# Performance work log

Measured on AMD Instinct MI355X. Metric: run time of the kernel, lower is better.

## Reference

```python
import jax, jax.numpy as jnp
import numpy as np

N_SRC = 100000
N_DST = 100000
N_EDGES = 1250000
D_FEAT = 64
HIDDEN = 64
OUT = 128


def setup_inputs() -> dict:
    key = jax.random.key(0)
    ks = jax.random.split(key, 9)
    h_src = jax.random.normal(ks[0], (N_SRC, D_FEAT), dtype=jnp.float32)
    h_dst = jax.random.normal(ks[1], (N_DST, D_FEAT), dtype=jnp.float32)
    edge_weight = jax.random.uniform(ks[2], (N_EDGES,), dtype=jnp.float32)
    W1 = jax.random.normal(ks[3], (D_FEAT, HIDDEN), dtype=jnp.float32) / np.sqrt(D_FEAT)
    b1 = jnp.zeros((HIDDEN,), dtype=jnp.float32)
    W2 = jax.random.normal(ks[4], (HIDDEN + D_FEAT, OUT), dtype=jnp.float32) / np.sqrt(HIDDEN + D_FEAT)
    b2 = jnp.zeros((OUT,), dtype=jnp.float32)
    src_idx = jax.random.randint(ks[5], (N_EDGES,), 0, N_SRC, dtype=jnp.int32)
    dst_idx = jax.random.randint(ks[6], (N_EDGES,), 0, N_DST, dtype=jnp.int32)
    return {
        "h_src": h_src, "h_dst": h_dst, "edge_weight": edge_weight,
        "W1": W1, "b1": b1, "W2": W2, "b2": b2,
        "src_idx": src_idx, "dst_idx": dst_idx,
    }


def reference(h_src, h_dst, edge_weight, W1, b1, W2, b2, src_idx, dst_idx):
    # fc_1 with relu on source features: [N_src, H]
    hs = jax.nn.relu(h_src @ W1 + b1)
    # u_mul_e -> sum: edge-weighted scatter-sum into dst nodes
    msg = hs[src_idx] * edge_weight[:, None]                      # [E, H]
    vs = jax.ops.segment_sum(msg, dst_idx, num_segments=N_DST)    # [N_dst, H]
    # copy_e -> sum: per-dst sum of edge weights
    ws = jax.ops.segment_sum(edge_weight, dst_idx, num_segments=N_DST)  # [N_dst]
    ws = jnp.clip(ws, 1.0, None)[:, None]
    nv = vs / ws
    # fc_2 on concat([weighted-mean, h_dst]) with relu
    new = jax.nn.relu(jnp.concatenate([nv, h_dst], axis=-1) @ W2 + b2)
    # global L2 normalization (tf.norm over the full tensor)
    return new / jnp.linalg.norm(new)
```

## Files before the change

### kernel.cpp

```cpp
#include <hip/hip_runtime.h>

#define N_SRC   100000
#define N_DST   100000
#define N_EDGES 1250000
#define D_FEAT  64
#define HIDDEN  64
#define OUT_F   128

#define DPB    128
#define NBUK   782
#define NBLKA  160
#define CHUNK  ((N_EDGES + NBLKA - 1) / NBLKA)
#define NCNT   (NBUK * NBLKA)
#define NB_SC  ((NCNT + 511) / 512)
#define CAPD   2048
#define NT_FC1 782
#define NT_A   391
#define NT_C   (NT_FC1 - NT_A)

struct FC1SM {
    float Xs[128][33];
    float Ws[32][64];
};

__device__ __forceinline__ void fc1_tile(FC1SM& sm, int tile,
        const float* __restrict__ h_src, const float* __restrict__ W1,
        const float* __restrict__ b1, float* __restrict__ hs) {
    const int t  = threadIdx.x;
    const int tr = t >> 3;
    const int tc = t & 7;
    const int base = tile * 128;
    float acc[4][8] = {};

    #pragma unroll 1
    for (int kc = 0; kc < 2; ++kc) {
        const int koff = kc * 32;
        #pragma unroll
        for (int i = 0; i < 4; ++i) {
            int fid = i * 256 + t;
            int row = fid >> 3, q = fid & 7;
            int grow = base + row;
            float4 v = make_float4(0.f, 0.f, 0.f, 0.f);
            if (grow < N_SRC)
                v = *(const float4*)&h_src[(size_t)grow * 64 + koff + q * 4];
            sm.Xs[row][q * 4 + 0] = v.x; sm.Xs[row][q * 4 + 1] = v.y;
            sm.Xs[row][q * 4 + 2] = v.z; sm.Xs[row][q * 4 + 3] = v.w;
        }
        #pragma unroll
        for (int i = 0; i < 2; ++i) {
            int fid = i * 256 + t;
            int kk = fid >> 4, q = fid & 15;
            float4 v = *(const float4*)&W1[(size_t)(koff + kk) * HIDDEN + q * 4];
            *(float4*)&sm.Ws[kk][q * 4] = v;
        }
        __syncthreads();
        #pragma unroll 2
        for (int k = 0; k < 32; ++k) {
            float xv[4];
            #pragma unroll
            for (int r = 0; r < 4; ++r) xv[r] = sm.Xs[tr * 4 + r][k];
            const float4 wlo = *(const float4*)&sm.Ws[k][tc * 8];
            const float4 whi = *(const float4*)&sm.Ws[k][tc * 8 + 4];
            #pragma unroll
            for (int r = 0; r < 4; ++r) {
                acc[r][0] = fmaf(xv[r], wlo.x, acc[r][0]);
                acc[r][1] = fmaf(xv[r], wlo.y, acc[r][1]);
                acc[r][2] = fmaf(xv[r], wlo.z, acc[r][2]);
                acc[r][3] = fmaf(xv[r], wlo.w, acc[r][3]);
                acc[r][4] = fmaf(xv[r], whi.x, acc[r][4]);
                acc[r][5] = fmaf(xv[r], whi.y, acc[r][5]);
                acc[r][6] = fmaf(xv[r], whi.z, acc[r][6]);
                acc[r][7] = fmaf(xv[r], whi.w, acc[r][7]);
            }
        }
        __syncthreads();
    }
    #pragma unroll
    for (int r = 0; r < 4; ++r) {
        int grow = base + tr * 4 + r;
        if (grow < N_SRC) {
            #pragma unroll
            for (int j = 0; j < 8; ++j)
                hs[(size_t)grow * 64 + tc * 8 + j] =
                    fmaxf(acc[r][j] + b1[tc * 8 + j], 0.0f);
        }
    }
}

__global__ __launch_bounds__(256, 4) void fusedA_kernel(
        const int* __restrict__ dst, int* __restrict__ bcnt,
        const float* __restrict__ h_src, const float* __restrict__ W1,
        const float* __restrict__ b1, float* __restrict__ hs) {
    __shared__ union { int h[NBUK]; FC1SM g; } sm;
    if (blockIdx.x >= NBLKA) {
        fc1_tile(sm.g, blockIdx.x - NBLKA, h_src, W1, b1, hs);
        return;
    }
    for (int i = threadIdx.x; i < NBUK; i += 256) sm.h[i] = 0;
    __syncthreads();
    const int lo = blockIdx.x * CHUNK;
    const int hi = min(lo + CHUNK, N_EDGES);
    for (int i = lo + threadIdx.x; i < hi; i += 256)
        atomicAdd(&sm.h[dst[i] >> 7], 1);
    __syncthreads();
    for (int b = threadIdx.x; b < NBUK; b += 256)
        bcnt[b * NBLKA + blockIdx.x] = sm.h[b];
}

__global__ __launch_bounds__(256) void scan_bsum_kernel(
        const int* __restrict__ c, int* __restrict__ bsum, int n) {
    const int t  = threadIdx.x;
    const int i0 = blockIdx.x * 512 + 2 * t;
    int v0 = (i0     < n) ? c[i0]     : 0;
    int v1 = (i0 + 1 < n) ? c[i0 + 1] : 0;
    int s = v0 + v1;
    #pragma unroll
    for (int off = 32; off > 0; off >>= 1) s += __shfl_down(s, off, 64);
    __shared__ int ws[4];
    if ((t & 63) == 0) ws[t >> 6] = s;
    __syncthreads();
    if (t == 0) bsum[blockIdx.x] = ws[0] + ws[1] + ws[2] + ws[3];
}

__global__ __launch_bounds__(256) void scan_boff_kernel(
        const int* __restrict__ bsum, int* __restrict__ boff, int nb) {
    const int t = threadIdx.x, lane = t & 63, w = t >> 6;
    int v = (t < nb) ? bsum[t] : 0;
    int inc = v;
    #pragma unroll
    for (int off = 1; off < 64; off <<= 1) {
        int u = __shfl_up(inc, off, 64);
        if (lane >= off) inc += u;
    }
    __shared__ int wsum[4];
    if (lane == 63) wsum[w] = inc;
    __syncthreads();
    int add = 0;
    for (int i = 0; i < w; ++i) add += wsum[i];
    if (t < nb) boff[t] = add + inc - v;
}

__global__ __launch_bounds__(256) void scan_write_kernel(
        const int* __restrict__ boff, int* __restrict__ c, int n) {
    const int t = threadIdx.x, lane = t & 63, w = t >> 6;
    const int i0 = blockIdx.x * 512 + 2 * t;
    int v0 = (i0     < n) ? c[i0]     : 0;
    int v1 = (i0 + 1 < n) ? c[i0 + 1] : 0;
    int s = v0 + v1;
    int inc = s;
    #pragma unroll
    for (int off = 1; off < 64; off <<= 1) {
        int u = __shfl_up(inc, off, 64);
        if (lane >= off) inc += u;
    }
    __shared__ int wsum[4];
    if (lane == 63) wsum[w] = inc;
    __syncthreads();
    int add = boff[blockIdx.x];
    for (int i = 0; i < w; ++i) add += wsum[i];
    int g = add + inc - s;
    if (i0     < n) c[i0]     = g;
    if (i0 + 1 < n) c[i0 + 1] = g + v0;
}

__global__ __launch_bounds__(256, 4) void fusedC_kernel(
        const int* __restrict__ src, const int* __restrict__ dst,
        const float* __restrict__ ew, const int* __restrict__ bofs,
        int2* __restrict__ bucketed,
        const float* __restrict__ h_src, const float* __restrict__ W1,
        const float* __restrict__ b1, float* __restrict__ hs) {
    __shared__ union { int cur[NBUK]; FC1SM g; } sm;
    if (blockIdx.x >= NBLKA) {
        fc1_tile(sm.g, blockIdx.x - NBLKA + NT_A, h_src, W1, b1, hs);
        return;
    }
    for (int b = threadIdx.x; b < NBUK; b += 256)
        sm.cur[b] = bofs[b * NBLKA + blockIdx.x];
    __syncthreads();
    const int lo = blockIdx.x * CHUNK;
    const int hi = min(lo + CHUNK, N_EDGES);
    for (int i = lo + threadIdx.x; i < hi; i += 256) {
        int d = dst[i];
        int b = d >> 7;
        int pos = atomicAdd(&sm.cur[b], 1);
        bucketed[pos] = make_int2(src[i] | ((d & 127) << 17), __float_as_int(ew[i]));
    }
}

__global__ __launch_bounds__(256) void bucketD_kernel(
        const float* __restrict__ hs, const int2* __restrict__ bucketed,
        const int* __restrict__ bofs, float* __restrict__ nv) {
    __shared__ int  cnt[DPB];
    __shared__ int  beg[DPB];
    __shared__ int  ofs[DPB];
    __shared__ int2 sorted[CAPD];
    const int b = blockIdx.x;
    const int t = threadIdx.x;
    const int s = bofs[b * NBLKA];
    const int e = (b + 1 < NBUK) ? bofs[(b + 1) * NBLKA] : N_EDGES;
    const int m = min(e - s, CAPD);

    for (int i = t; i < DPB; i += 256) cnt[i] = 0;
    __syncthreads();
    for (int i = t; i < m; i += 256)
        atomicAdd(&cnt[(bucketed[s + i].x >> 17) & 127], 1);
    __syncthreads();
    if (t < 64) {
        int a0 = cnt[2 * t], a1 = cnt[2 * t + 1];
        int sp = a0 + a1;
        int inc = sp;
        #pragma unroll
        for (int off = 1; off < 64; off <<= 1) {
            int u = __shfl_up(inc, off, 64);
            if (t >= off) inc += u;
        }
        int excl = inc - sp;
        beg[2 * t] = excl;      beg[2 * t + 1] = excl + a0;
        ofs[2 * t] = excl;      ofs[2 * t + 1] = excl + a0;
    }
    __syncthreads();
    for (int i = t; i < m; i += 256) {
        int2 en = bucketed[s + i];
        int p = atomicAdd(&ofs[(en.x >> 17) & 127], 1);
        sorted[p] = en;
    }
    __syncthreads();

    const int lane = t & 63;
    const int wv   = t >> 6;
    for (int j = wv; j < DPB; j += 4) {
        int d = b * DPB + j;
        if (d >= N_DST) continue;
        int lo = beg[j];
        const int hi = ofs[j];
        float acc = 0.0f, wsum = 0.0f;
        for (; lo + 3 < hi; lo += 4) {
            int2 p0 = sorted[lo],     p1 = sorted[lo + 1];
            int2 p2 = sorted[lo + 2], p3 = sorted[lo + 3];
            float w0 = __int_as_float(p0.y), w1 = __int_as_float(p1.y);
            float w2 = __int_as_float(p2.y), w3 = __int_as_float(p3.y);
            float h0 = hs[(size_t)(p0.x & 0x1FFFF) * 64 + lane];
            float h1 = hs[(size_t)(p1.x & 0x1FFFF) * 64 + lane];
            float h2 = hs[(size_t)(p2.x & 0x1FFFF) * 64 + lane];
            float h3 = hs[(size_t)(p3.x & 0x1FFFF) * 64 + lane];
            acc = fmaf(h0, w0, acc);
            acc = fmaf(h1, w1, acc);
            acc = fmaf(h2, w2, acc);
            acc = fmaf(h3, w3, acc);
            wsum += (w0 + w1) + (w2 + w3);
        }
        for (; lo < hi; ++lo) {
            int2 p = sorted[lo];
            float w0 = __int_as_float(p.y);
            acc = fmaf(hs[(size_t)(p.x & 0x1FFFF) * 64 + lane], w0, acc);
            wsum += w0;
        }
        nv[(size_t)d * 64 + lane] = acc / fmaxf(wsum, 1.0f);
    }
}

__global__ __launch_bounds__(256) void fc2_kernel(
        const float* __restrict__ nv, const float* __restrict__ h_dst,
        const float* __restrict__ W2, const float* __restrict__ b2,
        float* __restrict__ out, double* __restrict__ sumsq) {
    __shared__ float Xt[32][132];
    __shared__ float Ws[32][128];
    const int t  = threadIdx.x;
    const int tr = t >> 4;
    const int tc = t & 15;
    const int base = blockIdx.x * 128;
    float acc[8][8] = {};

    #pragma unroll 1
    for (int kc = 0; kc < 4; ++kc) {
        const float* __restrict__ xsrc = (kc < 2) ? nv : h_dst;
        const int koff = (kc & 1) * 32;
        #pragma unroll
        for (int i = 0; i < 4; ++i) {
            int fid = i * 256 + t;
            int row = fid >> 3, q = fid & 7;
            int grow = base + row;
            float4 v = make_float4(0.f, 0.f, 0.f, 0.f);
            if (grow < N_DST)
                v = *(const float4*)&xsrc[(size_t)grow * 64 + koff + q * 4];
            Xt[q * 4 + 0][row] = v.x;
            Xt[q * 4 + 1][row] = v.y;
            Xt[q * 4 + 2][row] = v.z;
            Xt[q * 4 + 3][row] = v.w;
        }
        #pragma unroll
        for (int i = 0; i < 4; ++i) {
            int fid = i * 256 + t;
            int kk = fid >> 5, q = fid & 31;
            float4 v = *(const float4*)&W2[(size_t)(kc * 32 + kk) * OUT_F + q * 4];
            *(float4*)&Ws[kk][q * 4] = v;
        }
        __syncthreads();
        #pragma unroll 2
        for (int k = 0; k < 32; ++k) {
            const float4 xa = *(const float4*)&Xt[k][tr * 8];
            const float4 xb = *(const float4*)&Xt[k][tr * 8 + 4];
            const float4 wa = *(const float4*)&Ws[k][tc * 4];
            const float4 wb = *(const float4*)&Ws[k][64 + tc * 4];
            float xr[8] = {xa.x, xa.y, xa.z, xa.w, xb.x, xb.y, xb.z, xb.w};
            #pragma unroll
            for (int r = 0; r < 8; ++r) {
                acc[r][0] = fmaf(xr[r], wa.x, acc[r][0]);
                acc[r][1] = fmaf(xr[r], wa.y, acc[r][1]);
                acc[r][2] = fmaf(xr[r], wa.z, acc[r][2]);
                acc[r][3] = fmaf(xr[r], wa.w, acc[r][3]);
                acc[r][4] = fmaf(xr[r], wb.x, acc[r][4]);
                acc[r][5] = fmaf(xr[r], wb.y, acc[r][5]);
                acc[r][6] = fmaf(xr[r], wb.z, acc[r][6]);
                acc[r][7] = fmaf(xr[r], wb.w, acc[r][7]);
            }
        }
        __syncthreads();
    }

    double ss = 0.0;
    #pragma unroll
    for (int r = 0; r < 8; ++r) {
        int grow = base + tr * 8 + r;
        if (grow < N_DST) {
            #pragma unroll
            for (int j = 0; j < 4; ++j) {
                float vA = fmaxf(acc[r][j]     + b2[tc * 4 + j],      0.0f);
                float vB = fmaxf(acc[r][j + 4] + b2[64 + tc * 4 + j], 0.0f);
                out[(size_t)grow * OUT_F + tc * 4 + j]      = vA;
                out[(size_t)grow * OUT_F + 64 + tc * 4 + j] = vB;
                ss += (double)vA * vA + (double)vB * vB;
            }
        }
    }
    #pragma unroll
    for (int off = 32; off > 0; off >>= 1) ss += __shfl_down(ss, off, 64);
    if ((t & 63) == 0) atomicAdd(sumsq, ss);
}

__global__ __launch_bounds__(256) void scale_kernel(
        float* __restrict__ out, const double* __restrict__ sumsq, int n4) {
    const float s = (float)(1.0 / sqrt(*sumsq));
    float4* o4 = (float4*)out;
    const int stride = gridDim.x * blockDim.x;
    for (int i = blockIdx.x * blockDim.x + threadIdx.x; i < n4; i += stride) {
        float4 v = o4[i];
        v.x *= s; v.y *= s; v.z *= s; v.w *= s;
        o4[i] = v;
    }
}

extern "C" void kernel_launch(void* const* d_in, const int* in_sizes, int n_in,
                              void* d_out, int out_size, void* d_ws, size_t ws_size,
                              hipStream_t stream) {
    const float* h_src = (const float*)d_in[0];
    const float* h_dst = (const float*)d_in[1];
    const float* ew    = (const float*)d_in[2];
    const float* W1    = (const float*)d_in[3];
    const float* b1    = (const float*)d_in[4];
    const float* W2    = (const float*)d_in[5];
    const float* b2    = (const float*)d_in[6];
    const int*   src   = (const int*)d_in[7];
    const int*   dst   = (const int*)d_in[8];
    float* out = (float*)d_out;

    float*  hs       = out;
    int2*   bucketed = (int2*)((char*)d_out + 25600000);
    int*    bcnt     = (int*)((char*)d_out + 35600000);
    int*    bsum2    = (int*)((char*)d_out + 36104192);
    int*    boff2    = (int*)((char*)d_out + 36105728);
    float*  nv       = (float*)d_ws;
    double* sumsq    = (double*)((char*)d_ws + 25600000);

    hipMemsetAsync(sumsq, 0, 8, stream);

    fusedA_kernel<<<NBLKA + NT_A, 256, 0, stream>>>(dst, bcnt, h_src, W1, b1, hs);
    scan_bsum_kernel<<<NB_SC, 256, 0, stream>>>(bcnt, bsum2, NCNT);
    scan_boff_kernel<<<1, 256, 0, stream>>>(bsum2, boff2, NB_SC);
    scan_write_kernel<<<NB_SC, 256, 0, stream>>>(boff2, bcnt, NCNT);
    fusedC_kernel<<<NBLKA + NT_C, 256, 0, stream>>>(src, dst, ew, bcnt, bucketed,
                                                    h_src, W1, b1, hs);
    bucketD_kernel<<<NBUK, 256, 0, stream>>>(hs, bucketed, bcnt, nv);
    fc2_kernel<<<(N_DST + 127) / 128, 256, 0, stream>>>(nv, h_dst, W2, b2, out, sumsq);
    scale_kernel<<<2048, 256, 0, stream>>>(out, sumsq, N_DST * OUT_F / 4);
}
```

Baseline: 214.2 us.

## Run fc2 on bf16 MFMA with split hi/lo precision emulation

Rewrites the fc2 GEMM to use 16x16x32 bf16 MFMA instructions in place of scalar FP32 FMAs. Three products (hi*hi, lo*hi, hi*lo) approximate FP32 accuracy. nv is now written as bf16 hi/lo pairs by the aggregation kernel. W2 is pre-split and transposed by extra blocks added to the first fused kernel. This moves the dense matmul onto matrix cores, at the cost of extra conversion work, small accuracy loss, and smaller 64-row tiles.

```diff
diff --git a/kernel.cpp b/kernel.cpp
--- a/kernel.cpp
+++ b/kernel.cpp
@@ -17,6 +17,23 @@
 #define NT_FC1 782
 #define NT_A   391
 #define NT_C   (NT_FC1 - NT_A)
+#define NB_W2T 8
+
+typedef __attribute__((ext_vector_type(8))) short s8v;
+typedef __attribute__((ext_vector_type(4))) float f4v;
+
+__device__ __forceinline__ unsigned short bf16_hi(float x) {
+    return (unsigned short)(__float_as_uint(x) >> 16);
+}
+__device__ __forceinline__ float bf16_hif(float x) {
+    return __uint_as_float(__float_as_uint(x) & 0xffff0000u);
+}
+__device__ __forceinline__ unsigned short bf16_lo(float x) {
+    return (unsigned short)(__float_as_uint(x - bf16_hif(x)) >> 16);
+}
+__device__ __forceinline__ unsigned int pack2(unsigned short a, unsigned short b) {
+    return (unsigned int)a | ((unsigned int)b << 16);
+}
 
 struct FC1SM {
     float Xs[128][33];
@@ -90,8 +107,22 @@
 __global__ __launch_bounds__(256, 4) void fusedA_kernel(
         const int* __restrict__ dst, int* __restrict__ bcnt,
         const float* __restrict__ h_src, const float* __restrict__ W1,
-        const float* __restrict__ b1, float* __restrict__ hs) {
+        const float* __restrict__ b1, float* __restrict__ hs,
+        const float* __restrict__ W2,
+        unsigned short* __restrict__ wth, unsigned short* __restrict__ wtl) {
     __shared__ union { int h[NBUK]; FC1SM g; } sm;
+    if (blockIdx.x >= NBLKA + NT_A) {
+        int i0 = (blockIdx.x - NBLKA - NT_A) * 2048 + threadIdx.x * 8;
+        #pragma unroll
+        for (int i = 0; i < 8; ++i) {
+            int idx = i0 + i;
+            int k = idx >> 7, c = idx & 127;
+            float x = W2[idx];
+            wth[c * 128 + k] = bf16_hi(x);
+            wtl[c * 128 + k] = bf16_lo(x);
+        }
+        return;
+    }
     if (blockIdx.x >= NBLKA) {
         fc1_tile(sm.g, blockIdx.x - NBLKA, h_src, W1, b1, hs);
         return;
@@ -189,7 +220,8 @@
 
 __global__ __launch_bounds__(256) void bucketD_kernel(
         const float* __restrict__ hs, const int2* __restrict__ bucketed,
-        const int* __restrict__ bofs, float* __restrict__ nv) {
+        const int* __restrict__ bofs,
+        unsigned short* __restrict__ nvh, unsigned short* __restrict__ nvl) {
     __shared__ int  cnt[DPB];
     __shared__ int  beg[DPB];
     __shared__ int  ofs[DPB];
@@ -255,92 +287,112 @@
             acc = fmaf(hs[(size_t)(p.x & 0x1FFFF) * 64 + lane], w0, acc);
             wsum += w0;
         }
-        nv[(size_t)d * 64 + lane] = acc / fmaxf(wsum, 1.0f);
+        float v = acc / fmaxf(wsum, 1.0f);
+        nvh[(size_t)d * 64 + lane] = bf16_hi(v);
+        nvl[(size_t)d * 64 + lane] = bf16_lo(v);
     }
 }
 
 __global__ __launch_bounds__(256) void fc2_kernel(
-        const float* __restrict__ nv, const float* __restrict__ h_dst,
-        const float* __restrict__ W2, const float* __restrict__ b2,
+        const unsigned short* __restrict__ nvh,
+        const unsigned short* __restrict__ nvl,
+        const float* __restrict__ h_dst,
+        const unsigned short* __restrict__ wth,
+        const unsigned short* __restrict__ wtl,
+        const float* __restrict__ b2,
         float* __restrict__ out, double* __restrict__ sumsq) {
-    __shared__ float Xt[32][132];
-    __shared__ float Ws[32][128];
-    const int t  = threadIdx.x;
-    const int tr = t >> 4;
-    const int tc = t & 15;
-    const int base = blockIdx.x * 128;
-    float acc[8][8] = {};
+    __shared__ unsigned short Xh[64][40], Xl[64][40];
+    __shared__ unsigned short Wh[128][40], Wl[128][40];
+    const int t    = threadIdx.x;
+    const int lane = t & 63;
+    const int w    = t >> 6;
+    const int base = blockIdx.x * 64;
+    const int rl   = lane & 15;
+    const int kq   = lane >> 4;
+    f4v acc[8];
+    #pragma unroll
+    for (int ct = 0; ct < 8; ++ct) acc[ct] = (f4v){0.f, 0.f, 0.f, 0.f};
 
     #pragma unroll 1
     for (int kc = 0; kc < 4; ++kc) {
-        const float* __restrict__ xsrc = (kc < 2) ? nv : h_dst;
-        const int koff = (kc & 1) * 32;
-        #pragma unroll
-        for (int i = 0; i < 4; ++i) {
-            int fid = i * 256 + t;
-            int row = fid >> 3, q = fid & 7;
+        {
+            int row = t >> 2, seg = t & 3;
             int grow = base + row;
-            float4 v = make_float4(0.f, 0.f, 0.f, 0.f);
-            if (grow < N_DST)
-                v = *(const float4*)&xsrc[(size_t)grow * 64 + koff + q * 4];
-            Xt[q * 4 + 0][row] = v.x;
-            Xt[q * 4 + 1][row] = v.y;
-            Xt[q * 4 + 2][row] = v.z;
-            Xt[q * 4 + 3][row] = v.w;
-        }
-        #pragma unroll
-        for (int i = 0; i < 4; ++i) {
-            int fid = i * 256 + t;
-            int kk = fid >> 5, q = fid & 31;
-            float4 v = *(const float4*)&W2[(size_t)(kc * 32 + kk) * OUT_F + q * 4];
-            *(float4*)&Ws[kk][q * 4] = v;
+            if (kc < 2) {
+                size_t off = (size_t)grow * 64 + kc * 32 + seg * 8;
+                uint4 vh = make_uint4(0, 0, 0, 0), vl = make_uint4(0, 0, 0, 0);
+                if (grow < N_DST) {
+                    vh = *(const uint4*)&nvh[off];
+                    vl = *(const uint4*)&nvl[off];
+                }
+                *(uint4*)&Xh[row][seg * 8] = vh;
+                *(uint4*)&Xl[row][seg * 8] = vl;
+            } else {
+                size_t off = (size_t)grow * 64 + (kc - 2) * 32 + seg * 8;
+                float4 a = make_float4(0.f, 0.f, 0.f, 0.f);
+                float4 b = make_float4(0.f, 0.f, 0.f, 0.f);
+                if (grow < N_DST) {
+                    a = *(const float4*)&h_dst[off];
+                    b = *(const float4*)&h_dst[off + 4];
+                }
+                uint4 vh = make_uint4(pack2(bf16_hi(a.x), bf16_hi(a.y)),
+                                      pack2(bf16_hi(a.z), bf16_hi(a.w)),
+                                      pack2(bf16_hi(b.x), bf16_hi(b.y)),
+                                      pack2(bf16_hi(b.z), bf16_hi(b.w)));
+                uint4 vl = make_uint4(pack2(bf16_lo(a.x), bf16_lo(a.y)),
+                                      pack2(bf16_lo(a.z), bf16_lo(a.w)),
+                                      pack2(bf16_lo(b.x), bf16_lo(b.y)),
+                                      pack2(bf16_lo(b.z), bf16_lo(b.w)));
+                *(uint4*)&Xh[row][seg * 8] = vh;
+                *(uint4*)&Xl[row][seg * 8] = vl;
+            }
+        }
+        {
+            int col = t >> 1, seg = t & 1;
+            size_t off = (size_t)col * 128 + kc * 32 + seg * 16;
+            *(uint4*)&Wh[col][seg * 16]     = *(const uint4*)&wth[off];
+            *(uint4*)&Wh[col][seg * 16 + 8] = *(const uint4*)&wth[off + 8];
+            *(uint4*)&Wl[col][seg * 16]     = *(const uint4*)&wtl[off];
+            *(uint4*)&Wl[col][seg * 16 + 8] = *(const uint4*)&wtl[off + 8];
         }
         __syncthreads();
-        #pragma unroll 2
-        for (int k = 0; k < 32; ++k) {
-            const float4 xa = *(const float4*)&Xt[k][tr * 8];
-            const float4 xb = *(const float4*)&Xt[k][tr * 8 + 4];
-            const float4 wa = *(const float4*)&Ws[k][tc * 4];
-            const float4 wb = *(const float4*)&Ws[k][64 + tc * 4];
-            float xr[8] = {xa.x, xa.y, xa.z, xa.w, xb.x, xb.y, xb.z, xb.w};
-            #pragma unroll
-            for (int r = 0; r < 8; ++r) {
-                acc[r][0] = fmaf(xr[r], wa.x, acc[r][0]);
-                acc[r][1] = fmaf(xr[r], wa.y, acc[r][1]);
-                acc[r][2] = fmaf(xr[r], wa.z, acc[r][2]);
-                acc[r][3] = fmaf(xr[r], wa.w, acc[r][3]);
-                acc[r][4] = fmaf(xr[r], wb.x, acc[r][4]);
-                acc[r][5] = fmaf(xr[r], wb.y, acc[r][5]);
-                acc[r][6] = fmaf(xr[r], wb.z, acc[r][6]);
-                acc[r][7] = fmaf(xr[r], wb.w, acc[r][7]);
+        s8v ah = *(const s8v*)&Xh[w * 16 + rl][kq * 8];
+        s8v al = *(const s8v*)&Xl[w * 16 + rl][kq * 8];
+        #pragma unroll
+        for (int ct = 0; ct < 8; ++ct) {
+            s8v bh = *(const s8v*)&Wh[ct * 16 + rl][kq * 8];
+            s8v bl = *(const s8v*)&Wl[ct * 16 + rl][kq * 8];
+            acc[ct] = __builtin_amdgcn_mfma_f32_16x16x32_bf16(ah, bh, acc[ct], 0, 0, 0);
+            acc[ct] = __builtin_amdgcn_mfma_f32_16x16x32_bf16(al, bh, acc[ct], 0, 0, 0);
+            acc[ct] = __builtin_amdgcn_mfma_f32_16x16x32_bf16(ah, bl, acc[ct], 0, 0, 0);
+        }
+        __syncthreads();
+    }
+
+    double ss = 0.0;
+    #pragma unroll
+    for (int ct = 0; ct < 8; ++ct) {
+        int col = ct * 16 + rl;
+        float bias = b2[col];
+        #pragma unroll
+        for (int r = 0; r < 4; ++r) {
+            int grow = base + w * 16 + kq * 4 + r;
+            if (grow < N_DST) {
+                float v = fmaxf(acc[ct][r] + bias, 0.0f);
+                out[(size_t)grow * OUT_F + col] = v;
+                ss += (double)v * (double)v;
             }
         }
-        __syncthreads();
-    }
-
-    double ss = 0.0;
-    #pragma unroll
-    for (int r = 0; r < 8; ++r) {
-        int grow = base + tr * 8 + r;
-        if (grow < N_DST) {
-            #pragma unroll
-            for (int j = 0; j < 4; ++j) {
-                float vA = fmaxf(acc[r][j]     + b2[tc * 4 + j],      0.0f);
-                float vB = fmaxf(acc[r][j + 4] + b2[64 + tc * 4 + j], 0.0f);
-                out[(size_t)grow * OUT_F + tc * 4 + j]      = vA;
-                out[(size_t)grow * OUT_F + 64 + tc * 4 + j] = vB;
-                ss += (double)vA * vA + (double)vB * vB;
-            }
-        }
     }
     #pragma unroll
     for (int off = 32; off > 0; off >>= 1) ss += __shfl_down(ss, off, 64);
-    if ((t & 63) == 0) atomicAdd(sumsq, ss);
+    if (lane == 0) atomicAdd(sumsq, ss);
 }
 
 __global__ __launch_bounds__(256) void scale_kernel(
         float* __restrict__ out, const double* __restrict__ sumsq, int n4) {
-    const float s = (float)(1.0 / sqrt(*sumsq));
+    const double q = *sumsq;
+    const float s = (q > 0.0) ? (float)(1.0 / sqrt(q)) : 0.0f;
     float4* o4 = (float4*)out;
     const int stride = gridDim.x * blockDim.x;
     for (int i = blockIdx.x * blockDim.x + threadIdx.x; i < n4; i += stride) {
@@ -369,18 +421,23 @@
     int*    bcnt     = (int*)((char*)d_out + 35600000);
     int*    bsum2    = (int*)((char*)d_out + 36104192);
     int*    boff2    = (int*)((char*)d_out + 36105728);
-    float*  nv       = (float*)d_ws;
+    unsigned short* nvh = (unsigned short*)d_ws;
+    unsigned short* nvl = (unsigned short*)((char*)d_ws + 12800000);
     double* sumsq    = (double*)((char*)d_ws + 25600000);
+    unsigned short* wth = (unsigned short*)((char*)d_ws + 25700000);
+    unsigned short* wtl = (unsigned short*)((char*)d_ws + 25800000);
 
     hipMemsetAsync(sumsq, 0, 8, stream);
 
-    fusedA_kernel<<<NBLKA + NT_A, 256, 0, stream>>>(dst, bcnt, h_src, W1, b1, hs);
+    fusedA_kernel<<<NBLKA + NT_A + NB_W2T, 256, 0, stream>>>(
+        dst, bcnt, h_src, W1, b1, hs, W2, wth, wtl);
     scan_bsum_kernel<<<NB_SC, 256, 0, stream>>>(bcnt, bsum2, NCNT);
     scan_boff_kernel<<<1, 256, 0, stream>>>(bsum2, boff2, NB_SC);
     scan_write_kernel<<<NB_SC, 256, 0, stream>>>(boff2, bcnt, NCNT);
     fusedC_kernel<<<NBLKA + NT_C, 256, 0, stream>>>(src, dst, ew, bcnt, bucketed,
                                                     h_src, W1, b1, hs);
-    bucketD_kernel<<<NBUK, 256, 0, stream>>>(hs, bucketed, bcnt, nv);
-    fc2_kernel<<<(N_DST + 127) / 128, 256, 0, stream>>>(nv, h_dst, W2, b2, out, sumsq);
+    bucketD_kernel<<<NBUK, 256, 0, stream>>>(hs, bucketed, bcnt, nvh, nvl);
+    fc2_kernel<<<(N_DST + 63) / 64, 256, 0, stream>>>(nvh, nvl, h_dst,
+                                                      wth, wtl, b2, out, sumsq);
     scale_kernel<<<2048, 256, 0, stream>>>(out, sumsq, N_DST * OUT_F / 4);
 }
```

Measured after the change: 245.0 us. 1.14x slower.
